# Optimization experiments

Measured on AMD Instinct MI355X. Metric: run time of the kernel, lower is better.

## Reference

```python
import jax, jax.numpy as jnp
import numpy as np

N = 16384; E = 262144; B = 8
IN = 768; HID = 256; H1 = 4; OUT = 128; H2 = 2

def setup_inputs() -> dict:
    key = jax.random.key(0)
    ks = jax.random.split(key, 16)
    s = 0.02
    def p(k, shape):
        return jax.random.normal(k, shape, jnp.float32) * s
    return {
        "x": jax.random.normal(ks[0], (N, IN), jnp.float32),
        "edge_index": jax.random.randint(ks[1], (2, E), 0, N),
        "batch": jnp.sort(jax.random.randint(ks[2], (N,), 0, B)),
        "W1": p(ks[3], (H1 * HID, IN)),
        "a_src1": p(ks[4], (H1, HID)),
        "a_dst1": p(ks[5], (H1, HID)),
        "b1": jnp.zeros((H1 * HID,), jnp.float32),
        "W2": p(ks[6], (H2 * OUT, H1 * HID)),
        "a_src2": p(ks[7], (H2, OUT)),
        "a_dst2": p(ks[8], (H2, OUT)),
        "b2": jnp.zeros((OUT,), jnp.float32),
        "proj_W": p(ks[9], (768, OUT)),
        "proj_b": jnp.zeros((768,), jnp.float32),
        "ln_g": jnp.ones((768,), jnp.float32),
        "ln_b": jnp.zeros((768,), jnp.float32),
        "rh_W1": p(ks[10], (32, OUT + 2)),
        "rh_b1": jnp.zeros((32,), jnp.float32),
        "rh_W2": p(ks[11], (1, 32)),
        "rh_b2": jnp.zeros((1,), jnp.float32),
        "num_graphs": B,
    }

def _gat(x, src, dst, W, a_s, a_d, bias, heads, ch, concat, n):
    # PyG GATConv (shared src/dst lin): h = x W^T -> [n, heads, ch]
    h = (x @ W.T).reshape(n, heads, ch)
    al_s = (h * a_s).sum(-1)  # [n, heads]
    al_d = (h * a_d).sum(-1)
    e = jax.nn.leaky_relu(al_s[src] + al_d[dst], 0.2)  # [E', heads]
    # segment softmax over incoming edges of each destination node
    m = jax.lax.stop_gradient(jax.ops.segment_max(e, dst, num_segments=n))
    ex = jnp.exp(e - m[dst])
    den = jax.ops.segment_sum(ex, dst, num_segments=n)
    w = ex / (den[dst] + 1e-16)
    out = jax.ops.segment_sum(w[:, :, None] * h[src], dst, num_segments=n)
    if concat:
        return out.reshape(n, heads * ch) + bias
    return out.mean(1) + bias

def reference(x, edge_index, batch, W1, a_src1, a_dst1, b1, W2, a_src2, a_dst2, b2,
              proj_W, proj_b, ln_g, ln_b, rh_W1, rh_b1, rh_W2, rh_b2, num_graphs):
    n = x.shape[0]
    src0, dst0 = edge_index[0], edge_index[1]
    loop = jnp.arange(n)  # GATConv adds self-loops by default
    src = jnp.concatenate([src0, loop])
    dst = jnp.concatenate([dst0, loop])
    h1 = jax.nn.elu(_gat(x, src, dst, W1, a_src1, a_dst1, b1, H1, HID, True, n))
    h2 = jax.nn.elu(_gat(h1, src, dst, W2, a_src2, a_dst2, b2, H2, OUT, False, n))
    # global mean pool per graph
    n_g = jax.ops.segment_sum(jnp.ones((n,), x.dtype), batch, num_segments=num_graphs)
    pooled = jax.ops.segment_sum(h2, batch, num_segments=num_graphs) / jnp.maximum(n_g, 1.0)[:, None]
    pe = pooled @ proj_W.T + proj_b
    mu = pe.mean(-1, keepdims=True)
    var = pe.var(-1, keepdims=True)
    struct_embed = (pe - mu) / jnp.sqrt(var + 1e-5) * ln_g + ln_b
    # topology stats from ORIGINAL edges (no self-loops), per original code
    e_g = jax.ops.segment_sum(jnp.ones((src0.shape[0],), x.dtype), batch[src0], num_segments=num_graphs)
    stats = jnp.stack([e_g / (n_g + 1e-6), jnp.log(n_g + 1.0)], axis=-1)  # [B, 2]
    ri = jnp.concatenate([pooled, stats], axis=-1)
    hid = jax.nn.relu(ri @ rh_W1.T + rh_b1)
    prop_risk = jax.nn.sigmoid(hid @ rh_W2.T + rh_b2)[:, 0]
    return struct_embed, h2, prop_risk
```

## Files before the change

### kernel.cpp

```cpp
#include <hip/hip_runtime.h>
#include <math.h>

#define NN    16384
#define EE    262144
#define ET    (EE + NN)
#define NB    8
#define IN_F  768
#define HID1  256
#define H1    4
#define D1    (H1*HID1)
#define OUT2  128
#define H2    2
#define D2    (H2*OUT2)

typedef __attribute__((ext_vector_type(8))) _Float16 f16x8;
typedef __attribute__((ext_vector_type(4))) float f32x4;

__device__ __forceinline__ float hf2f(unsigned short u) {
    union { unsigned short u; _Float16 h; } c; c.u = u; return (float)c.h;
}
__device__ __forceinline__ unsigned short f2hf(float f) {
    union { unsigned short u; _Float16 h; } c; c.h = (_Float16)f; return c.u;
}


__global__ void hist_kernel(const int* __restrict__ ei, const int* __restrict__ batch,
                            int* __restrict__ deg, int* __restrict__ n_g, int* __restrict__ e_cnt) {
    __shared__ int le[NB], ln[NB];
    int tid = threadIdx.x;
    if (tid < NB) { le[tid] = 0; ln[tid] = 0; }
    __syncthreads();
    int t = blockIdx.x * blockDim.x + tid;
    if (t < EE) {
        int s = ei[t];
        int d = ei[EE + t];
        atomicAdd(&deg[d], 1);
        atomicAdd(&le[batch[s]], 1);
    }
    if (t < NN) {
        atomicAdd(&ln[batch[t]], 1);
    }
    __syncthreads();
    if (tid < NB) {
        if (le[tid]) atomicAdd(&e_cnt[tid], le[tid]);
        if (ln[tid]) atomicAdd(&n_g[tid], ln[tid]);
    }
}

__global__ __launch_bounds__(1024) void scan_kernel(const int* __restrict__ deg, int* __restrict__ row_ptr) {
    __shared__ int sums[1024];
    int t = threadIdx.x;
    int base = t * 16;
    int local[16];
    int acc = 0;
#pragma unroll
    for (int i = 0; i < 16; i++) { local[i] = acc; acc += deg[base + i] + 1; }
    sums[t] = acc;
    __syncthreads();
    for (int off = 1; off < 1024; off <<= 1) {
        int v = (t >= off) ? sums[t - off] : 0;
        __syncthreads();
        sums[t] += v;
        __syncthreads();
    }
    int prev = (t == 0) ? 0 : sums[t - 1];
#pragma unroll
    for (int i = 0; i < 16; i++) row_ptr[base + i] = prev + local[i];
    if (t == 1023) row_ptr[NN] = sums[1023];
}

__global__ void scatter_kernel(const int* __restrict__ ei, const int* __restrict__ row_ptr,
                               int* __restrict__ cursor, int* __restrict__ colidx) {
    int t = blockIdx.x * blockDim.x + threadIdx.x;
    if (t >= ET) return;
    int s, d;
    if (t < EE) { s = ei[t]; d = ei[EE + t]; }
    else        { s = d = t - EE; }
    int pos = row_ptr[d] + atomicAdd(&cursor[d], 1);
    colidx[pos] = s;
}


__global__ void tohalf_kernel(const float* __restrict__ in, unsigned short* __restrict__ o, int n4) {
    int i = blockIdx.x * blockDim.x + threadIdx.x;
    if (i >= n4) return;
    float4 v = ((const float4*)in)[i];
    ushort4 h;
    h.x = f2hf(v.x); h.y = f2hf(v.y); h.z = f2hf(v.z); h.w = f2hf(v.w);
    ((ushort4*)o)[i] = h;
}


__device__ __forceinline__ void ld_lds16(const unsigned short* g, unsigned short* l) {
    __builtin_amdgcn_global_load_lds((__attribute__((address_space(1))) void*)g,
                                     (__attribute__((address_space(3))) void*)l, 16, 0, 0);
}

#define BM 128
#define BN 128
#define BK 32

__global__ __launch_bounds__(256) void gemm_mfma(const unsigned short* __restrict__ A,
                                                 const unsigned short* __restrict__ B,
                                                 unsigned short* __restrict__ C,
                                                 int M, int N, int K) {
    __shared__ __align__(16) unsigned short sA[BM * BK];
    __shared__ __align__(16) unsigned short sB[BN * BK];
    int t = threadIdx.x;
    int lane = t & 63, wave = t >> 6;

    int NC = N / BN;
    int b = blockIdx.x;
    int xcd = b & 7;
    int idx = b >> 3;
    int c = idx % NC;
    int rg = idx / NC;
    int bm = (rg * 8 + xcd) * BM;
    int bn = c * BN;

    int wm = (wave & 1) * 64, wn = (wave >> 1) * 64;

    const unsigned short* gbase;
    unsigned short* lbase;
    {
        int hrow = (wave & 1) * 64;
        if (wave < 2) { gbase = A + (size_t)(bm + hrow) * K; lbase = sA + hrow * BK; }
        else          { gbase = B + (size_t)(bn + hrow) * K; lbase = sB + hrow * BK; }
    }
    int schunk = (lane & 3) ^ ((lane >> 3) & 3);
    const unsigned short* gsrc = gbase + (size_t)(lane >> 2) * K + schunk * 8;

    f32x4 zero = {0.f, 0.f, 0.f, 0.f};
    f32x4 acc[4][4];
#pragma unroll
    for (int i = 0; i < 4; i++)
#pragma unroll
        for (int j = 0; j < 4; j++) acc[i][j] = zero;

    int row16 = lane & 15;
    int kq = ((lane >> 4) ^ ((row16 >> 1) & 3)) * 8;

    for (int k0 = 0; k0 < K; k0 += BK) {
#pragma unroll
        for (int i = 0; i < 4; i++)
            ld_lds16(gsrc + k0 + (size_t)(i * 16) * K, lbase + i * 16 * BK);
        __syncthreads();

        f16x8 ah[4], bh[4];
#pragma unroll
        for (int mt = 0; mt < 4; mt++)
            ah[mt] = *(const f16x8*)&sA[(wm + mt * 16 + row16) * BK + kq];
#pragma unroll
        for (int nt = 0; nt < 4; nt++)
            bh[nt] = *(const f16x8*)&sB[(wn + nt * 16 + row16) * BK + kq];
#pragma unroll
        for (int mt = 0; mt < 4; mt++)
#pragma unroll
            for (int nt = 0; nt < 4; nt++)
                acc[mt][nt] = __builtin_amdgcn_mfma_f32_16x16x32_f16(ah[mt], bh[nt], acc[mt][nt], 0, 0, 0);
        __syncthreads();
    }

    int crow0 = bm + wm + (lane >> 4) * 4;
    int ccol0 = bn + wn + row16;
#pragma unroll
    for (int mt = 0; mt < 4; mt++)
#pragma unroll
        for (int nt = 0; nt < 4; nt++)
#pragma unroll
            for (int reg = 0; reg < 4; reg++)
                C[(size_t)(crow0 + mt * 16 + reg) * N + ccol0 + nt * 16] = f2hf(acc[mt][nt][reg]);
}


template <int H, int CH>
__global__ void al_kernel(const unsigned short* __restrict__ h, const float* __restrict__ a_s,
                          const float* __restrict__ a_d, float* __restrict__ als,
                          float* __restrict__ ald) {
    int node = blockIdx.x;
    int wave = threadIdx.x >> 6;
    int lane = threadIdx.x & 63;
    const unsigned short* row = h + (size_t)node * (H * CH) + wave * CH;
    float ss = 0.f, sd = 0.f;
#pragma unroll
    for (int c = lane; c < CH; c += 64) {
        float v = hf2f(row[c]);
        ss += v * a_s[wave * CH + c];
        sd += v * a_d[wave * CH + c];
    }
#pragma unroll
    for (int off = 32; off; off >>= 1) {
        ss += __shfl_down(ss, off);
        sd += __shfl_down(sd, off);
    }
    if (lane == 0) {
        als[node * H + wave] = ss;
        ald[node * H + wave] = sd;
    }
}

__device__ __forceinline__ float leaky(float v) { return v > 0.f ? v : 0.2f * v; }
__device__ __forceinline__ float elu1(float v) { return v > 0.f ? v : (__expf(v) - 1.f); }


__global__ __launch_bounds__(256) void agg1_kernel(const unsigned short* __restrict__ h,
                                                   const float* __restrict__ als,
                                                   const float* __restrict__ ald,
                                                   const int* __restrict__ row_ptr,
                                                   const int* __restrict__ colidx,
                                                   const float* __restrict__ bias,
                                                   unsigned short* __restrict__ outp) {
    int b = blockIdx.x;
    int s = b & 7;
    int g = b >> 3;
    int wave = threadIdx.x >> 6;
    int lane = threadIdx.x & 63;
    int lanesel = lane & 32;
    int l5 = lane & 31;
    int d = g * 8 + wave * 2 + (lanesel >> 5);
    int head = s >> 1;
    int start = row_ptr[d], end = row_ptr[d + 1];
    int deg = end - start;
    int degO = __shfl_xor(deg, 32);
    int degmax = max(deg, degO);
    float ald_h = ald[d * H1 + head];
    unsigned choff = (unsigned)(s * 128 + l5 * 4);

    float a0 = 0.f, a1 = 0.f, a2 = 0.f, a3 = 0.f;
    float wsum = 0.f;

    for (int c0 = 0; c0 < degmax; c0 += 32) {
        int ee = start + c0 + l5;
        int idx = ee < end ? ee : end - 1;
        int sL = colidx[idx];
        float ev = leaky(als[(sL << 2) + head] + ald_h);
        float wL = (ee < end) ? __expf(ev) : 0.f;
        float ws = wL;
        ws += __shfl_xor(ws, 16); ws += __shfl_xor(ws, 8);
        ws += __shfl_xor(ws, 4);  ws += __shfl_xor(ws, 2);  ws += __shfl_xor(ws, 1);
        wsum += ws;

        int n = degmax - c0; if (n > 32) n = 32;
        int n8 = (n + 7) & ~7;
        for (int k = 0; k < n8; k += 8) {
            ushort4 hv[8]; float wv[8];
#pragma unroll
            for (int j = 0; j < 8; j++) {
                int src = k + j + lanesel;
                int ssj = __shfl(sL, src);
                wv[j]   = __shfl(wL, src);
                hv[j] = *(const ushort4*)(h + (((unsigned)ssj << 10) + choff));
            }
#pragma unroll
            for (int j = 0; j < 8; j++) {
                float w = wv[j];
                a0 += w * hf2f(hv[j].x); a1 += w * hf2f(hv[j].y);
                a2 += w * hf2f(hv[j].z); a3 += w * hf2f(hv[j].w);
            }
        }
    }

    float sinv = 1.f / (wsum + 1e-16f);
    float4 bv = *(const float4*)(bias + s * 128 + l5 * 4);
    float o0 = elu1(a0 * sinv + bv.x);
    float o1 = elu1(a1 * sinv + bv.y);
    float o2 = elu1(a2 * sinv + bv.z);
    float o3 = elu1(a3 * sinv + bv.w);
    unsigned long long pk = (unsigned long long)f2hf(o0)
                          | ((unsigned long long)f2hf(o1) << 16)
                          | ((unsigned long long)f2hf(o2) << 32)
                          | ((unsigned long long)f2hf(o3) << 48);
    size_t o = (size_t)d * D1 + choff;
    __builtin_nontemporal_store(pk, (unsigned long long*)(outp + o));
}


__global__ __launch_bounds__(256) void agg2_kernel(const unsigned short* __restrict__ h,
                                                   const float* __restrict__ als,
                                                   const float* __restrict__ ald,
                                                   const int* __restrict__ row_ptr,
                                                   const int* __restrict__ colidx,
                                                   const float* __restrict__ bias,
                                                   float* __restrict__ out) {
    int wave = threadIdx.x >> 6;
    int lane = threadIdx.x & 63;
    int lanesel = lane & 32;
    int l5 = lane & 31;
    int head = lanesel >> 5;
    int d = blockIdx.x * 4 + wave;
    int start = row_ptr[d], end = row_ptr[d + 1];
    int deg = end - start;
    float ald_h = ald[d * H2 + head];
    unsigned ch4 = (unsigned)(lane << 2);

    float a0 = 0.f, a1 = 0.f, a2 = 0.f, a3 = 0.f;
    float wsum = 0.f;

    for (int c0 = 0; c0 < deg; c0 += 32) {
        int ee = start + c0 + l5;
        int idx = ee < end ? ee : end - 1;
        int sL = colidx[idx];
        float ev = leaky(als[(sL << 1) + head] + ald_h);
        float wL = (ee < end) ? __expf(ev) : 0.f;
        float ws = wL;
        ws += __shfl_xor(ws, 16); ws += __shfl_xor(ws, 8);
        ws += __shfl_xor(ws, 4);  ws += __shfl_xor(ws, 2);  ws += __shfl_xor(ws, 1);
        wsum += ws;

        int n = deg - c0; if (n > 32) n = 32;
        int n8 = (n + 7) & ~7;
        for (int k = 0; k < n8; k += 8) {
            ushort4 hv[8]; float wv[8];
#pragma unroll
            for (int j = 0; j < 8; j++) {
                int ssj = __builtin_amdgcn_readlane(sL, k + j);
                wv[j] = __shfl(wL, k + j + lanesel);
                hv[j] = *(const ushort4*)(h + (((unsigned)ssj << 8) + ch4));
            }
#pragma unroll
            for (int j = 0; j < 8; j++) {
                float w = wv[j];
                a0 += w * hf2f(hv[j].x); a1 += w * hf2f(hv[j].y);
                a2 += w * hf2f(hv[j].z); a3 += w * hf2f(hv[j].w);
            }
        }
    }

    float sinv = 1.f / (wsum + 1e-16f);
    float r0 = a0 * sinv, r1 = a1 * sinv, r2 = a2 * sinv, r3 = a3 * sinv;
    r0 += __shfl_xor(r0, 32);
    r1 += __shfl_xor(r1, 32);
    r2 += __shfl_xor(r2, 32);
    r3 += __shfl_xor(r3, 32);
    if (lane < 32) {
        float4 bv = *(const float4*)(bias + (l5 << 2));
        float4 o;
        o.x = elu1(r0 * 0.5f + bv.x);
        o.y = elu1(r1 * 0.5f + bv.y);
        o.z = elu1(r2 * 0.5f + bv.z);
        o.w = elu1(r3 * 0.5f + bv.w);
        *(float4*)(out + (size_t)d * OUT2 + (l5 << 2)) = o;
    }
}


__global__ __launch_bounds__(256) void pool_kernel(const float* __restrict__ h2,
                                                   const int* __restrict__ batch,
                                                   float* __restrict__ pooled) {
    int c = threadIdx.x & 127;
    int half = threadIdx.x >> 7;
    int n0 = blockIdx.x * 256 + half;
    int nend = blockIdx.x * 256 + 256;
    float acc = 0.f;
    int curg = batch[n0];
    for (int n = n0; n < nend; n += 2) {
        int g = batch[n];
        if (g != curg) {
            atomicAdd(&pooled[curg * OUT2 + c], acc);
            acc = 0.f; curg = g;
        }
        acc += h2[(size_t)n * OUT2 + c];
    }
    atomicAdd(&pooled[curg * OUT2 + c], acc);
}


__global__ __launch_bounds__(256) void final_kernel(const float* __restrict__ pooled_sum,
                                                    const int* __restrict__ n_g_i,
                                                    const int* __restrict__ e_cnt,
                                                    const float* __restrict__ projW,
                                                    const float* __restrict__ projb,
                                                    const float* __restrict__ lng,
                                                    const float* __restrict__ lnb,
                                                    const float* __restrict__ rhW1,
                                                    const float* __restrict__ rhb1,
                                                    const float* __restrict__ rhW2,
                                                    const float* __restrict__ rhb2,
                                                    float* __restrict__ out_se,
                                                    float* __restrict__ out_risk) {
    int b = blockIdx.x;
    int t = threadIdx.x;
    __shared__ float pooled[OUT2];
    __shared__ float pe[768];
    __shared__ float red[256];
    __shared__ float hid[32];
    __shared__ float stat_mu, stat_inv;

    float ng = (float)n_g_i[b];
    if (t < OUT2) pooled[t] = pooled_sum[b * OUT2 + t] / fmaxf(ng, 1.0f);
    __syncthreads();

    for (int j = t; j < 768; j += 256) {
        const float* wr = projW + (size_t)j * OUT2;
        float s = projb[j];
        for (int c = 0; c < OUT2; c++) s += pooled[c] * wr[c];
        pe[j] = s;
    }
    __syncthreads();

    float ls = 0.f, lq = 0.f;
    for (int j = t; j < 768; j += 256) { float v = pe[j]; ls += v; lq += v * v; }
    red[t] = ls;
    __syncthreads();
    for (int off = 128; off; off >>= 1) { if (t < off) red[t] += red[t + off]; __syncthreads(); }
    float tot = red[0];
    __syncthreads();
    red[t] = lq;
    __syncthreads();
    for (int off = 128; off; off >>= 1) { if (t < off) red[t] += red[t + off]; __syncthreads(); }
    float totq = red[0];
    if (t == 0) {
        float mu = tot / 768.f;
        float var = totq / 768.f - mu * mu;
        stat_mu = mu;
        stat_inv = 1.f / sqrtf(var + 1e-5f);
    }
    __syncthreads();
    float mu = stat_mu, inv = stat_inv;
    for (int j = t; j < 768; j += 256)
        out_se[(size_t)b * 768 + j] = (pe[j] - mu) * inv * lng[j] + lnb[j];

    float s0 = (float)e_cnt[b] / (ng + 1e-6f);
    float s1 = logf(ng + 1.0f);
    if (t < 32) {
        const float* wr = rhW1 + t * (OUT2 + 2);
        float s = rhb1[t];
        for (int c = 0; c < OUT2; c++) s += pooled[c] * wr[c];
        s += s0 * wr[OUT2] + s1 * wr[OUT2 + 1];
        hid[t] = fmaxf(s, 0.f);
    }
    __syncthreads();
    if (t == 0) {
        float s = rhb2[0];
        for (int k = 0; k < 32; k++) s += hid[k] * rhW2[k];
        out_risk[b] = 1.f / (1.f + __expf(-s));
    }
}


extern "C" void kernel_launch(void* const* d_in, const int* in_sizes, int n_in,
                              void* d_out, int out_size, void* d_ws, size_t ws_size,
                              hipStream_t stream) {
    const float* x     = (const float*)d_in[0];
    const int*   ei    = (const int*)  d_in[1];
    const int*   batch = (const int*)  d_in[2];
    const float* W1    = (const float*)d_in[3];
    const float* a_s1  = (const float*)d_in[4];
    const float* a_d1  = (const float*)d_in[5];
    const float* b1    = (const float*)d_in[6];
    const float* W2    = (const float*)d_in[7];
    const float* a_s2  = (const float*)d_in[8];
    const float* a_d2  = (const float*)d_in[9];
    const float* b2    = (const float*)d_in[10];
    const float* projW = (const float*)d_in[11];
    const float* projb = (const float*)d_in[12];
    const float* lng   = (const float*)d_in[13];
    const float* lnb   = (const float*)d_in[14];
    const float* rhW1  = (const float*)d_in[15];
    const float* rhb1  = (const float*)d_in[16];
    const float* rhW2  = (const float*)d_in[17];
    const float* rhb2  = (const float*)d_in[18];

    char* ws = (char*)d_ws;
    size_t off = 0;
    auto alloc = [&](size_t bytes) -> void* {
        void* p = ws + off;
        off += (bytes + 255) & ~(size_t)255;
        return p;
    };

    unsigned short* regionA = (unsigned short*)alloc((size_t)NN * D1 * 2);
    unsigned short* x_f  = regionA;
    unsigned short* h1a  = regionA;

    unsigned short* h1f  = (unsigned short*)alloc((size_t)NN * D1 * 2);
    unsigned short* h2ft = (unsigned short*)alloc((size_t)NN * D2 * 2);
    unsigned short* W1f  = (unsigned short*)alloc((size_t)D1 * IN_F * 2);
    unsigned short* W2f  = (unsigned short*)alloc((size_t)D2 * D1 * 2);
    float* als1   = (float*)alloc((size_t)NN * H1 * 4);
    float* ald1   = (float*)alloc((size_t)NN * H1 * 4);
    float* als2   = (float*)alloc((size_t)NN * H2 * 4);
    float* ald2   = (float*)alloc((size_t)NN * H2 * 4);
    int*   row_ptr= (int*)  alloc((size_t)(NN + 1) * 4);
    int*   colidx = (int*)  alloc((size_t)ET * 4);
    size_t zoff = off;
    int*   deg    = (int*)  alloc((size_t)NN * 4);
    int*   cursor = (int*)  alloc((size_t)NN * 4);
    int*   n_g    = (int*)  alloc((size_t)NB * 4);
    int*   e_cnt  = (int*)  alloc((size_t)NB * 4);
    float* pooled = (float*)alloc((size_t)NB * OUT2 * 4);
    size_t zbytes = off - zoff;

    float* out_se   = (float*)d_out;
    float* h2out    = out_se + NB * 768;
    float* out_risk = h2out + (size_t)NN * OUT2;

    hipMemsetAsync(ws + zoff, 0, zbytes, stream);

    hist_kernel<<<(EE + 255) / 256, 256, 0, stream>>>(ei, batch, deg, n_g, e_cnt);
    scan_kernel<<<1, 1024, 0, stream>>>(deg, row_ptr);
    scatter_kernel<<<(ET + 255) / 256, 256, 0, stream>>>(ei, row_ptr, cursor, colidx);

    tohalf_kernel<<<((NN * IN_F / 4) + 255) / 256, 256, 0, stream>>>(x, x_f, NN * IN_F / 4);
    tohalf_kernel<<<((D1 * IN_F / 4) + 255) / 256, 256, 0, stream>>>(W1, W1f, D1 * IN_F / 4);
    tohalf_kernel<<<((D2 * D1 / 4) + 255) / 256, 256, 0, stream>>>(W2, W2f, D2 * D1 / 4);

    gemm_mfma<<<(NN / BM) * (D1 / BN), 256, 0, stream>>>(x_f, W1f, h1f, NN, D1, IN_F);
    al_kernel<H1, HID1><<<NN, H1 * 64, 0, stream>>>(h1f, a_s1, a_d1, als1, ald1);
    agg1_kernel<<<NN, 256, 0, stream>>>(h1f, als1, ald1, row_ptr, colidx, b1, h1a);

    gemm_mfma<<<(NN / BM) * (D2 / BN), 256, 0, stream>>>(h1a, W2f, h2ft, NN, D2, D1);
    al_kernel<H2, OUT2><<<NN, H2 * 64, 0, stream>>>(h2ft, a_s2, a_d2, als2, ald2);
    agg2_kernel<<<NN / 4, 256, 0, stream>>>(h2ft, als2, ald2, row_ptr, colidx, b2, h2out);

    pool_kernel<<<NN / 256, 256, 0, stream>>>(h2out, batch, pooled);

    final_kernel<<<NB, 256, 0, stream>>>(pooled, n_g, e_cnt, projW, projb, lng, lnb,
                                         rhW1, rhb1, rhW2, rhb2, out_se, out_risk);
}
```

Baseline: 406.0 us.

## Precompute edge softmax weights and inverse sums in separate kernel

Adds a wcalc kernel per GAT layer that computes exp(leaky(als[src]+ald[dst])) for all heads per edge, stores them in CSR order, and writes the inverse softmax denominator per node and head. The aggregation kernels then read precomputed weights instead of gathering als, computing exp and doing shuffle reductions, which removes redundant work repeated across the 8 channel-slice blocks per node in agg1. In exchange it adds two kernel launches and writes and rereads about 4.5 MB and 2.2 MB of edge weights.

Measured after the change: 412.3 us. No clear change (+1.6%).

```diff
diff --git a/kernel.cpp b/kernel.cpp
--- a/kernel.cpp
+++ b/kernel.cpp
@@ -203,9 +203,74 @@
 __device__ __forceinline__ float elu1(float v) { return v > 0.f ? v : (__expf(v) - 1.f); }
 
 
+template <int H>
+__global__ __launch_bounds__(256) void wcalc_kernel(const float* __restrict__ als,
+                                                    const float* __restrict__ ald,
+                                                    const int* __restrict__ row_ptr,
+                                                    const int* __restrict__ colidx,
+                                                    float* __restrict__ w,
+                                                    float* __restrict__ sinv) {
+    int wave = threadIdx.x >> 6;
+    int lane = threadIdx.x & 63;
+    int l5 = lane & 31;
+    int d = blockIdx.x * 8 + wave * 2 + (lane >> 5);
+    int start = row_ptr[d], end = row_ptr[d + 1];
+    int deg = end - start;
+    int degO = __shfl_xor(deg, 32);
+    int degmax = max(deg, degO);
+    float aldl[H];
+#pragma unroll
+    for (int hh = 0; hh < H; hh++) aldl[hh] = ald[d * H + hh];
+    float wsum[H];
+#pragma unroll
+    for (int hh = 0; hh < H; hh++) wsum[hh] = 0.f;
+
+    for (int c0 = 0; c0 < degmax; c0 += 32) {
+        int ee = start + c0 + l5;
+        int idx = ee < end ? ee : end - 1;
+        int sL = colidx[idx];
+        float av[H];
+        if constexpr (H == 4) {
+            float4 a4 = *(const float4*)(als + (size_t)sL * 4);
+            av[0] = a4.x; av[1] = a4.y; av[2] = a4.z; av[3] = a4.w;
+        } else {
+            float2 a2 = *(const float2*)(als + (size_t)sL * 2);
+            av[0] = a2.x; av[1] = a2.y;
+        }
+        float wv[H];
+#pragma unroll
+        for (int hh = 0; hh < H; hh++) {
+            float ev = leaky(av[hh] + aldl[hh]);
+            wv[hh] = (ee < end) ? __expf(ev) : 0.f;
+        }
+#pragma unroll
+        for (int hh = 0; hh < H; hh++) {
+            float ws = wv[hh];
+            ws += __shfl_xor(ws, 16); ws += __shfl_xor(ws, 8);
+            ws += __shfl_xor(ws, 4);  ws += __shfl_xor(ws, 2);  ws += __shfl_xor(ws, 1);
+            wsum[hh] += ws;
+        }
+        if (ee < end) {
+            if constexpr (H == 4) {
+                float4 o = make_float4(wv[0], wv[1], wv[2], wv[3]);
+                *(float4*)(w + (size_t)ee * 4) = o;
+            } else {
+                float2 o = make_float2(wv[0], wv[1]);
+                *(float2*)(w + (size_t)ee * 2) = o;
+            }
+        }
+    }
+    if (l5 == 0) {
+#pragma unroll
+        for (int hh = 0; hh < H; hh++)
+            sinv[d * H + hh] = 1.f / (wsum[hh] + 1e-16f);
+    }
+}
+
+
 __global__ __launch_bounds__(256) void agg1_kernel(const unsigned short* __restrict__ h,
-                                                   const float* __restrict__ als,
-                                                   const float* __restrict__ ald,
+                                                   const float* __restrict__ w1,
+                                                   const float* __restrict__ sinv1,
                                                    const int* __restrict__ row_ptr,
                                                    const int* __restrict__ colidx,
                                                    const float* __restrict__ bias,
@@ -223,22 +288,16 @@
     int deg = end - start;
     int degO = __shfl_xor(deg, 32);
     int degmax = max(deg, degO);
-    float ald_h = ald[d * H1 + head];
+    float sinv = sinv1[d * H1 + head];
     unsigned choff = (unsigned)(s * 128 + l5 * 4);
 
     float a0 = 0.f, a1 = 0.f, a2 = 0.f, a3 = 0.f;
-    float wsum = 0.f;
 
     for (int c0 = 0; c0 < degmax; c0 += 32) {
         int ee = start + c0 + l5;
         int idx = ee < end ? ee : end - 1;
         int sL = colidx[idx];
-        float ev = leaky(als[(sL << 2) + head] + ald_h);
-        float wL = (ee < end) ? __expf(ev) : 0.f;
-        float ws = wL;
-        ws += __shfl_xor(ws, 16); ws += __shfl_xor(ws, 8);
-        ws += __shfl_xor(ws, 4);  ws += __shfl_xor(ws, 2);  ws += __shfl_xor(ws, 1);
-        wsum += ws;
+        float wL = (ee < end) ? w1[(size_t)idx * 4 + head] : 0.f;
 
         int n = degmax - c0; if (n > 32) n = 32;
         int n8 = (n + 7) & ~7;
@@ -260,7 +319,6 @@
         }
     }
 
-    float sinv = 1.f / (wsum + 1e-16f);
     float4 bv = *(const float4*)(bias + s * 128 + l5 * 4);
     float o0 = elu1(a0 * sinv + bv.x);
     float o1 = elu1(a1 * sinv + bv.y);
@@ -276,8 +334,8 @@
 
 
 __global__ __launch_bounds__(256) void agg2_kernel(const unsigned short* __restrict__ h,
-                                                   const float* __restrict__ als,
-                                                   const float* __restrict__ ald,
+                                                   const float* __restrict__ w2,
+                                                   const float* __restrict__ sinv2,
                                                    const int* __restrict__ row_ptr,
                                                    const int* __restrict__ colidx,
                                                    const float* __restrict__ bias,
@@ -290,22 +348,16 @@
     int d = blockIdx.x * 4 + wave;
     int start = row_ptr[d], end = row_ptr[d + 1];
     int deg = end - start;
-    float ald_h = ald[d * H2 + head];
+    float sinv = sinv2[d * H2 + head];
     unsigned ch4 = (unsigned)(lane << 2);
 
     float a0 = 0.f, a1 = 0.f, a2 = 0.f, a3 = 0.f;
-    float wsum = 0.f;
 
     for (int c0 = 0; c0 < deg; c0 += 32) {
         int ee = start + c0 + l5;
         int idx = ee < end ? ee : end - 1;
         int sL = colidx[idx];
-        float ev = leaky(als[(sL << 1) + head] + ald_h);
-        float wL = (ee < end) ? __expf(ev) : 0.f;
-        float ws = wL;
-        ws += __shfl_xor(ws, 16); ws += __shfl_xor(ws, 8);
-        ws += __shfl_xor(ws, 4);  ws += __shfl_xor(ws, 2);  ws += __shfl_xor(ws, 1);
-        wsum += ws;
+        float wL = (ee < end) ? w2[(size_t)idx * 2 + head] : 0.f;
 
         int n = deg - c0; if (n > 32) n = 32;
         int n8 = (n + 7) & ~7;
@@ -326,7 +378,6 @@
         }
     }
 
-    float sinv = 1.f / (wsum + 1e-16f);
     float r0 = a0 * sinv, r1 = a1 * sinv, r2 = a2 * sinv, r3 = a3 * sinv;
     r0 += __shfl_xor(r0, 32);
     r1 += __shfl_xor(r1, 32);
@@ -481,6 +532,10 @@
     float* ald1   = (float*)alloc((size_t)NN * H1 * 4);
     float* als2   = (float*)alloc((size_t)NN * H2 * 4);
     float* ald2   = (float*)alloc((size_t)NN * H2 * 4);
+    float* w1     = (float*)alloc((size_t)ET * H1 * 4);
+    float* sinv1  = (float*)alloc((size_t)NN * H1 * 4);
+    float* w2     = (float*)alloc((size_t)ET * H2 * 4);
+    float* sinv2  = (float*)alloc((size_t)NN * H2 * 4);
     int*   row_ptr= (int*)  alloc((size_t)(NN + 1) * 4);
     int*   colidx = (int*)  alloc((size_t)ET * 4);
     size_t zoff = off;
@@ -507,11 +562,13 @@
 
     gemm_mfma<<<(NN / BM) * (D1 / BN), 256, 0, stream>>>(x_f, W1f, h1f, NN, D1, IN_F);
     al_kernel<H1, HID1><<<NN, H1 * 64, 0, stream>>>(h1f, a_s1, a_d1, als1, ald1);
-    agg1_kernel<<<NN, 256, 0, stream>>>(h1f, als1, ald1, row_ptr, colidx, b1, h1a);
+    wcalc_kernel<H1><<<NN / 8, 256, 0, stream>>>(als1, ald1, row_ptr, colidx, w1, sinv1);
+    agg1_kernel<<<NN, 256, 0, stream>>>(h1f, w1, sinv1, row_ptr, colidx, b1, h1a);
 
     gemm_mfma<<<(NN / BM) * (D2 / BN), 256, 0, stream>>>(h1a, W2f, h2ft, NN, D2, D1);
     al_kernel<H2, OUT2><<<NN, H2 * 64, 0, stream>>>(h2ft, a_s2, a_d2, als2, ald2);
-    agg2_kernel<<<NN / 4, 256, 0, stream>>>(h2ft, als2, ald2, row_ptr, colidx, b2, h2out);
+    wcalc_kernel<H2><<<NN / 8, 256, 0, stream>>>(als2, ald2, row_ptr, colidx, w2, sinv2);
+    agg2_kernel<<<NN / 4, 256, 0, stream>>>(h2ft, w2, sinv2, row_ptr, colidx, b2, h2out);
 
     pool_kernel<<<NN / 256, 256, 0, stream>>>(h2out, batch, pooled);
 
```

## Fuse attention-logit dot products into GEMM epilogue and merge fp16 conversions

Applied to the files above, without the earlier changes.

The per-node attention logit kernels are removed. Each GEMM now computes the src/dst logit partial sums from its fp32 accumulators in the epilogue, reduces them across lanes with shuffles, and accumulates them into zeroed buffers with atomics. The three fp32-to-fp16 conversion launches are merged into one kernel. This removes a full re-read of the hidden features and several launches, at the cost of atomics, zeroing the logit buffers, and summation from unrounded accumulators, which differs slightly from summing the fp16-rounded values.

Result: no change. 413.6 us (+1.9%).

```diff
diff --git a/kernel.cpp b/kernel.cpp
--- a/kernel.cpp
+++ b/kernel.cpp
@@ -81,13 +81,22 @@
 }
 
 
-__global__ void tohalf_kernel(const float* __restrict__ in, unsigned short* __restrict__ o, int n4) {
+__global__ void tohalf3_kernel(const float* __restrict__ x,  unsigned short* __restrict__ xo,
+                               const float* __restrict__ w1, unsigned short* __restrict__ w1o,
+                               const float* __restrict__ w2, unsigned short* __restrict__ w2o) {
+    const int n1 = NN * IN_F / 4;
+    const int n2 = D1 * IN_F / 4;
+    const int n3 = D2 * D1 / 4;
     int i = blockIdx.x * blockDim.x + threadIdx.x;
-    if (i >= n4) return;
-    float4 v = ((const float4*)in)[i];
+    const float* src; unsigned short* dst; int j;
+    if (i < n1)           { src = x;  dst = xo;  j = i; }
+    else if (i < n1 + n2) { src = w1; dst = w1o; j = i - n1; }
+    else if (i < n1 + n2 + n3) { src = w2; dst = w2o; j = i - n1 - n2; }
+    else return;
+    float4 v = ((const float4*)src)[j];
     ushort4 h;
     h.x = f2hf(v.x); h.y = f2hf(v.y); h.z = f2hf(v.z); h.w = f2hf(v.w);
-    ((ushort4*)o)[i] = h;
+    ((ushort4*)dst)[j] = h;
 }
 
 
@@ -100,10 +109,15 @@
 #define BN 128
 #define BK 32
 
-__global__ __launch_bounds__(256) void gemm_mfma(const unsigned short* __restrict__ A,
-                                                 const unsigned short* __restrict__ B,
-                                                 unsigned short* __restrict__ C,
-                                                 int M, int N, int K) {
+template <int H, int CH>
+__global__ __launch_bounds__(256) void gemm_al(const unsigned short* __restrict__ A,
+                                               const unsigned short* __restrict__ B,
+                                               unsigned short* __restrict__ C,
+                                               const float* __restrict__ a_s,
+                                               const float* __restrict__ a_d,
+                                               float* __restrict__ als,
+                                               float* __restrict__ ald,
+                                               int M, int N, int K) {
     __shared__ __align__(16) unsigned short sA[BM * BK];
     __shared__ __align__(16) unsigned short sB[BN * BK];
     int t = threadIdx.x;
@@ -170,33 +184,33 @@
 #pragma unroll
             for (int reg = 0; reg < 4; reg++)
                 C[(size_t)(crow0 + mt * 16 + reg) * N + ccol0 + nt * 16] = f2hf(acc[mt][nt][reg]);
-}
-
-
-template <int H, int CH>
-__global__ void al_kernel(const unsigned short* __restrict__ h, const float* __restrict__ a_s,
-                          const float* __restrict__ a_d, float* __restrict__ als,
-                          float* __restrict__ ald) {
-    int node = blockIdx.x;
-    int wave = threadIdx.x >> 6;
-    int lane = threadIdx.x & 63;
-    const unsigned short* row = h + (size_t)node * (H * CH) + wave * CH;
-    float ss = 0.f, sd = 0.f;
-#pragma unroll
-    for (int c = lane; c < CH; c += 64) {
-        float v = hf2f(row[c]);
-        ss += v * a_s[wave * CH + c];
-        sd += v * a_d[wave * CH + c];
-    }
-#pragma unroll
-    for (int off = 32; off; off >>= 1) {
-        ss += __shfl_down(ss, off);
-        sd += __shfl_down(sd, off);
-    }
-    if (lane == 0) {
-        als[node * H + wave] = ss;
-        ald[node * H + wave] = sd;
-    }
+
+    int head = bn / CH;
+    float asv[4], adv[4];
+#pragma unroll
+    for (int nt = 0; nt < 4; nt++) {
+        asv[nt] = a_s[ccol0 + nt * 16];
+        adv[nt] = a_d[ccol0 + nt * 16];
+    }
+#pragma unroll
+    for (int mt = 0; mt < 4; mt++)
+#pragma unroll
+        for (int reg = 0; reg < 4; reg++) {
+            float ss = acc[mt][0][reg] * asv[0] + acc[mt][1][reg] * asv[1]
+                     + acc[mt][2][reg] * asv[2] + acc[mt][3][reg] * asv[3];
+            float sd = acc[mt][0][reg] * adv[0] + acc[mt][1][reg] * adv[1]
+                     + acc[mt][2][reg] * adv[2] + acc[mt][3][reg] * adv[3];
+#pragma unroll
+            for (int m = 8; m; m >>= 1) {
+                ss += __shfl_xor(ss, m);
+                sd += __shfl_xor(sd, m);
+            }
+            if (row16 == 0) {
+                int row = crow0 + mt * 16 + reg;
+                atomicAdd(&als[row * H + head], ss);
+                atomicAdd(&ald[row * H + head], sd);
+            }
+        }
 }
 
 __device__ __forceinline__ float leaky(float v) { return v > 0.f ? v : 0.2f * v; }
@@ -477,13 +491,13 @@
     unsigned short* h2ft = (unsigned short*)alloc((size_t)NN * D2 * 2);
     unsigned short* W1f  = (unsigned short*)alloc((size_t)D1 * IN_F * 2);
     unsigned short* W2f  = (unsigned short*)alloc((size_t)D2 * D1 * 2);
+    int*   row_ptr= (int*)  alloc((size_t)(NN + 1) * 4);
+    int*   colidx = (int*)  alloc((size_t)ET * 4);
+    size_t zoff = off;
     float* als1   = (float*)alloc((size_t)NN * H1 * 4);
     float* ald1   = (float*)alloc((size_t)NN * H1 * 4);
     float* als2   = (float*)alloc((size_t)NN * H2 * 4);
     float* ald2   = (float*)alloc((size_t)NN * H2 * 4);
-    int*   row_ptr= (int*)  alloc((size_t)(NN + 1) * 4);
-    int*   colidx = (int*)  alloc((size_t)ET * 4);
-    size_t zoff = off;
     int*   deg    = (int*)  alloc((size_t)NN * 4);
     int*   cursor = (int*)  alloc((size_t)NN * 4);
     int*   n_g    = (int*)  alloc((size_t)NB * 4);
@@ -501,16 +515,17 @@
     scan_kernel<<<1, 1024, 0, stream>>>(deg, row_ptr);
     scatter_kernel<<<(ET + 255) / 256, 256, 0, stream>>>(ei, row_ptr, cursor, colidx);
 
-    tohalf_kernel<<<((NN * IN_F / 4) + 255) / 256, 256, 0, stream>>>(x, x_f, NN * IN_F / 4);
-    tohalf_kernel<<<((D1 * IN_F / 4) + 255) / 256, 256, 0, stream>>>(W1, W1f, D1 * IN_F / 4);
-    tohalf_kernel<<<((D2 * D1 / 4) + 255) / 256, 256, 0, stream>>>(W2, W2f, D2 * D1 / 4);
-
-    gemm_mfma<<<(NN / BM) * (D1 / BN), 256, 0, stream>>>(x_f, W1f, h1f, NN, D1, IN_F);
-    al_kernel<H1, HID1><<<NN, H1 * 64, 0, stream>>>(h1f, a_s1, a_d1, als1, ald1);
+    {
+        int ntot = NN * IN_F / 4 + D1 * IN_F / 4 + D2 * D1 / 4;
+        tohalf3_kernel<<<(ntot + 255) / 256, 256, 0, stream>>>(x, x_f, W1, W1f, W2, W2f);
+    }
+
+    gemm_al<H1, HID1><<<(NN / BM) * (D1 / BN), 256, 0, stream>>>(x_f, W1f, h1f, a_s1, a_d1,
+                                                                 als1, ald1, NN, D1, IN_F);
     agg1_kernel<<<NN, 256, 0, stream>>>(h1f, als1, ald1, row_ptr, colidx, b1, h1a);
 
-    gemm_mfma<<<(NN / BM) * (D2 / BN), 256, 0, stream>>>(h1a, W2f, h2ft, NN, D2, D1);
-    al_kernel<H2, OUT2><<<NN, H2 * 64, 0, stream>>>(h2ft, a_s2, a_d2, als2, ald2);
+    gemm_al<H2, OUT2><<<(NN / BM) * (D2 / BN), 256, 0, stream>>>(h1a, W2f, h2ft, a_s2, a_d2,
+                                                                 als2, ald2, NN, D2, D1);
     agg2_kernel<<<NN / 4, 256, 0, stream>>>(h2ft, als2, ald2, row_ptr, colidx, b2, h2out);
 
     pool_kernel<<<NN / 256, 256, 0, stream>>>(h2out, batch, pooled);
```
